# Kernel tuning notes

Hardware: AMD Instinct MI355X
Metric: run time of the kernel (lower is better)

The kernel has to match this reference:

```python
import jax, jax.numpy as jnp
import numpy as np
from jax import lax

K = 3
PAD = 1

def setup_inputs() -> dict:
    key = jax.random.key(0)
    ks = jax.random.split(key, 5)
    B, C, H, W, O = 4, 128, 128, 128, 256
    x = jax.random.normal(ks[0], (B, C, H, W), dtype=jnp.float32)
    w_off = jax.random.normal(ks[1], (3 * K * K, C, K, K), dtype=jnp.float32) * 0.05
    b_off = jnp.zeros((3 * K * K,), dtype=jnp.float32)
    w_dw = jax.random.normal(ks[2], (C, 1, K, K), dtype=jnp.float32) * 0.2
    b_dw = jnp.zeros((C,), dtype=jnp.float32)
    w_pw = jax.random.normal(ks[3], (O, C), dtype=jnp.float32) * (1.0 / np.sqrt(C))
    b_pw = jnp.zeros((O,), dtype=jnp.float32)
    return {"x": x, "w_off": w_off, "b_off": b_off, "w_dw": w_dw,
            "b_dw": b_dw, "w_pw": w_pw, "b_pw": b_pw}

def _dcn_forward(x, w_off, b_off, w_dw, b_dw, w_pw, b_pw):
    B, C, H, W = x.shape
    K2 = K * K
    # offset/mask conv (stride 1, pad 1) -> [B, 3*K*K, H, W]
    om = lax.conv_general_dilated(
        x, w_off, window_strides=(1, 1), padding=[(PAD, PAD), (PAD, PAD)],
        dimension_numbers=("NCHW", "OIHW", "NCHW")) + b_off[None, :, None, None]
    off = om[:, : 2 * K2]                      # [B, 2*K2, H, W]
    mask = jax.nn.sigmoid(om[:, 2 * K2:])      # [B, K2, H, W]
    dy = off[:, 0::2]                          # [B, K2, H, W] (y offsets)
    dx = off[:, 1::2]                          # [B, K2, H, W] (x offsets)
    # base sampling grid per kernel tap
    ky, kx = jnp.meshgrid(jnp.arange(K), jnp.arange(K), indexing="ij")
    ky = (ky.reshape(-1) - PAD).astype(x.dtype)   # [K2]
    kx = (kx.reshape(-1) - PAD).astype(x.dtype)
    py = jnp.arange(H, dtype=x.dtype)[None, None, :, None] + ky[None, :, None, None] + dy
    px = jnp.arange(W, dtype=x.dtype)[None, None, None, :] + kx[None, :, None, None] + dx
    y0 = jnp.floor(py); x0 = jnp.floor(px)
    wy = py - y0;       wx = px - x0

    def gather(yc, xc):
        # yc, xc: [B, K2, H, W] float corner coords; zero outside bounds
        valid = ((yc >= 0) & (yc < H) & (xc >= 0) & (xc < W)).astype(x.dtype)
        yi = jnp.clip(yc, 0, H - 1).astype(jnp.int32)
        xi = jnp.clip(xc, 0, W - 1).astype(jnp.int32)
        idx = yi * W + xi                       # [B, K2, H, W]
        def per_b(xb, ib):
            # xb: [C, H, W]; ib: [K2, H, W] -> [C, K2, H, W]
            return jnp.take(xb.reshape(C, -1), ib.reshape(-1), axis=1).reshape(C, K2, H, W)
        v = jax.vmap(per_b)(x, idx)             # [B, C, K2, H, W]
        return v * valid[:, None]

    val = (gather(y0, x0) * ((1 - wy) * (1 - wx))[:, None]
           + gather(y0, x0 + 1) * ((1 - wy) * wx)[:, None]
           + gather(y0 + 1, x0) * (wy * (1 - wx))[:, None]
           + gather(y0 + 1, x0 + 1) * (wy * wx)[:, None])  # [B, C, K2, H, W]
    val = val * mask[:, None]
    # depthwise deformable conv: per-channel K2 weights
    wk = w_dw.reshape(C, K2)
    out = jnp.einsum("bckhw,ck->bchw", val, wk) + b_dw[None, :, None, None]
    # pointwise 1x1 conv
    out = jnp.einsum("bchw,oc->bohw", out, w_pw) + b_pw[None, :, None, None]
    return out

def reference(x, w_off, b_off, w_dw, b_dw, w_pw, b_pw):
    return _dcn_forward(x, w_off, b_off, w_dw, b_dw, w_pw, b_pw)
```

## Files before the change

### kernel.cpp

```cpp
#include <hip/hip_runtime.h>
#include <hip/hip_bf16.h>
#include <math.h>

#define BB 4
#define CC 128
#define HH 128
#define WW 128
#define OO 256
#define HWP 16384

typedef __attribute__((ext_vector_type(8))) _Float16 half8;
typedef __attribute__((ext_vector_type(2))) _Float16 half2t;
typedef __attribute__((ext_vector_type(4))) float floatx4;

__device__ inline half2t u2h2(unsigned int u) {
  union { unsigned int i; half2t h; } z; z.i = u; return z.h;
}
__device__ inline unsigned short f2h_bits(float f) {
  union { _Float16 h; unsigned short s; } z; z.h = (_Float16)f; return z.s;
}

__device__ inline void blend2(unsigned int a00w, unsigned int a01w,
                              unsigned int a10w, unsigned int a11w,
                              half2t wt, half2t wb, float wk0, float wk1,
                              float& acc0, float& acc1) {
  unsigned int tl = __builtin_amdgcn_perm(a01w, a00w, 0x05040100u);
  unsigned int th = __builtin_amdgcn_perm(a01w, a00w, 0x07060302u);
  unsigned int bl = __builtin_amdgcn_perm(a11w, a10w, 0x05040100u);
  unsigned int bh = __builtin_amdgcn_perm(a11w, a10w, 0x07060302u);
  float v0 = __builtin_amdgcn_fdot2(u2h2(bl), wb, __builtin_amdgcn_fdot2(u2h2(tl), wt, 0.f, false), false);
  float v1 = __builtin_amdgcn_fdot2(u2h2(bh), wb, __builtin_amdgcn_fdot2(u2h2(th), wt, 0.f, false), false);
  acc0 = fmaf(v0, wk0, acc0);
  acc1 = fmaf(v1, wk1, acc1);
}

__device__ inline int om_idx(int px, int o) {
  return (((o >> 2) ^ (px & 7)) << 2) | (o & 3);
}

__global__ __launch_bounds__(256) void k_transpose(const float* __restrict__ x,
                                                   const float* __restrict__ w_off,
                                                   const float* __restrict__ w_pw,
                                                   unsigned int* __restrict__ xh32,
                                                   _Float16* __restrict__ Ah,
                                                   _Float16* __restrict__ Apw) {
  int tid = threadIdx.x;
  if (blockIdx.z == 4) {
    int e = (blockIdx.x * 128 + blockIdx.y) * 256 + tid;
    if (e < 144 * 32 * 8) {
      int kblk = e >> 8;
      int o = (e >> 3) & 31;
      int j = e & 7;
      int k = kblk * 8 + j;
      int t = k >> 7, c = k & 127;
      float w = (o < 27) ? w_off[(o * CC + c) * 9 + t] : 0.0f;
      Ah[e] = (_Float16)w;
    }
    int e2 = e - 144 * 32 * 8;
    if (e2 >= 0 && e2 < 16 * 256 * 8) {
      int cblk = e2 >> 11;
      int o = (e2 >> 3) & 255;
      int j = e2 & 7;
      Apw[e2] = (_Float16)w_pw[o * CC + cblk * 8 + j];
    }
    return;
  }
  __shared__ float tile[32][132];
  int ct = blockIdx.x;
  int h = blockIdx.y, b = blockIdx.z;
  int f4 = tid & 31;
  int cl = tid >> 5;
#pragma unroll
  for (int i = 0; i < 4; i++) {
    int c = cl + i * 8;
    float4 v = *(const float4*)(x + ((size_t)(b * CC + ct * 32 + c) * HH + h) * WW + f4 * 4);
    *(float4*)&tile[c][f4 * 4] = v;
  }
  __syncthreads();
  int cg = tid & 3;
#pragma unroll
  for (int pass = 0; pass < 2; pass++) {
    int px = pass * 64 + (tid >> 2);
    unsigned int d0, d1, d2, d3;
    d0 = (unsigned int)f2h_bits(tile[cg * 8 + 0][px]) | ((unsigned int)f2h_bits(tile[cg * 8 + 1][px]) << 16);
    d1 = (unsigned int)f2h_bits(tile[cg * 8 + 2][px]) | ((unsigned int)f2h_bits(tile[cg * 8 + 3][px]) << 16);
    d2 = (unsigned int)f2h_bits(tile[cg * 8 + 4][px]) | ((unsigned int)f2h_bits(tile[cg * 8 + 5][px]) << 16);
    d3 = (unsigned int)f2h_bits(tile[cg * 8 + 6][px]) | ((unsigned int)f2h_bits(tile[cg * 8 + 7][px]) << 16);
    uint4 z; z.x = d0; z.y = d1; z.z = d2; z.w = d3;
    *(uint4*)(xh32 + (size_t)((b * HH + h) * WW + px) * 64 + ct * 16 + cg * 4) = z;
  }
}

__global__ __launch_bounds__(256, 4) void k_fused(
    const _Float16* __restrict__ xh, const _Float16* __restrict__ Ah,
    const _Float16* __restrict__ Apw, const float* __restrict__ b_off,
    const float* __restrict__ w_dw, const float* __restrict__ b_dw,
    const float* __restrict__ bpw, float* __restrict__ out) {
  __shared__ float om_s[64][32];
  __shared__ int s_packed[64][9];
  __shared__ unsigned int s_wp[64][9][2];
  __shared__ __align__(16) _Float16 val[64][128];

  int tid = threadIdx.x;
  int bid = blockIdx.x;
  int n0 = ((bid & 7) * 128 + (bid >> 3)) * 64;
  int b = n0 >> 14;
  int h0 = (n0 >> 7) & 127;
  int wbase = n0 & 127;

  int wv = tid >> 6, lane = tid & 63;
  int n16 = lane & 15, quad = lane >> 4;

  {
    int pxb = wv * 16;
    floatx4 acc0 = {}, acc1 = {};
    half8 zz = {};
#pragma unroll
    for (int t = 0; t < 9; t++) {
      int dy = t / 3 - 1, dx = t % 3 - 1;
      int hs = h0 + dy;
      bool hok = ((unsigned)hs < HH);
      int hsc = min(max(hs, 0), HH - 1);
      int wA = wbase + pxb + n16 + dx;
      bool okA = hok && ((unsigned)wA < WW);
      int wAc = min(max(wA, 0), WW - 1);
      size_t rowoff = (size_t)((b * HH + hsc) * WW + wAc) * CC + quad * 8;
#pragma unroll
      for (int cs = 0; cs < 4; cs++) {
        half8 bh = *(const half8*)(xh + rowoff + cs * 32);
        bh = okA ? bh : zz;
        int kblk = t * 16 + cs * 4 + quad;
        const _Float16* pa = Ah + (size_t)kblk * 256 + n16 * 8;
        half8 a0 = *(const half8*)pa;
        half8 a1 = *(const half8*)(pa + 128);
        __builtin_amdgcn_s_setprio(1);
        acc0 = __builtin_amdgcn_mfma_f32_16x16x32_f16(a0, bh, acc0, 0, 0, 0);
        acc1 = __builtin_amdgcn_mfma_f32_16x16x32_f16(a1, bh, acc1, 0, 0, 0);
        __builtin_amdgcn_s_setprio(0);
      }
    }
    int px = pxb + n16;
#pragma unroll
    for (int reg = 0; reg < 4; reg++) {
      int o0 = quad * 4 + reg;
      om_s[px][om_idx(px, o0)] = acc0[reg] + b_off[o0];
      int o1 = 16 + quad * 4 + reg;
      if (o1 < 27) om_s[px][om_idx(px, o1)] = acc1[reg] + b_off[o1];
    }
  }

#pragma unroll
  for (int pass = 0; pass < 3; pass++) {
    int it = pass * 64 + lane;
    if (it < 144) {
      int pxl = it / 9;
      int k = it - pxl * 9;
      int px = wv * 16 + pxl;
      int w = wbase + px;
      float dyv = om_s[px][om_idx(px, 2 * k)];
      float dxv = om_s[px][om_idx(px, 2 * k + 1)];
      float mvv = om_s[px][om_idx(px, 18 + k)];
      mvv = 1.0f / (1.0f + __expf(-mvv));
      float py = (float)(h0 + k / 3 - 1) + dyv;
      float pxf = (float)(w + k % 3 - 1) + dxv;
      float y0f = floorf(py), x0f = floorf(pxf);
      float wy = py - y0f, wx = pxf - x0f;
      int y0 = (int)y0f, x0 = (int)x0f;
      int y1 = y0 + 1, x1 = x0 + 1;
      float v00 = (y0 >= 0 && y0 < HH && x0 >= 0 && x0 < WW) ? 1.f : 0.f;
      float v01 = (y0 >= 0 && y0 < HH && x1 >= 0 && x1 < WW) ? 1.f : 0.f;
      float v10 = (y1 >= 0 && y1 < HH && x0 >= 0 && x0 < WW) ? 1.f : 0.f;
      float v11 = (y1 >= 0 && y1 < HH && x1 >= 0 && x1 < WW) ? 1.f : 0.f;
      int y0c = min(max(y0, 0), HH - 1), y1c = min(max(y1, 0), HH - 1);
      int x0c = min(max(x0, 0), WW - 1), x1c = min(max(x1, 0), WW - 1);
      int base = ((b * HH + y0c) * WW + x0c) * CC;
      int dxf = (x1c > x0c) ? 1 : 0;
      int dyf = (y1c > y0c) ? 1 : 0;
      s_packed[px][k] = base | (dxf << 30) | (dyf << 31);
      float w00 = (1.f - wy) * (1.f - wx) * mvv * v00;
      float w01 = (1.f - wy) * wx * mvv * v01;
      float w10 = wy * (1.f - wx) * mvv * v10;
      float w11 = wy * wx * mvv * v11;
      s_wp[px][k][0] = (unsigned int)f2h_bits(w00) | ((unsigned int)f2h_bits(w01) << 16);
      s_wp[px][k][1] = (unsigned int)f2h_bits(w10) | ((unsigned int)f2h_bits(w11) << 16);
    }
  }

  {
    int c0 = lane * 2;
    const unsigned short* xs = (const unsigned short*)xh;
    float wk0[9], wk1[9];
    {
      const float* wp_ = w_dw + c0 * 9;
#pragma unroll
      for (int k = 0; k < 9; k++) { wk0[k] = wp_[k]; wk1[k] = wp_[9 + k]; }
    }
    float2 bdp = *(const float2*)(b_dw + c0);

    unsigned int A00[9], A01[9], A10[9], A11[9];
    unsigned int B00[9], B01[9], B10[9], B11[9];

    auto issue = [&](int pxl, unsigned int* c00, unsigned int* c01,
                     unsigned int* c10, unsigned int* c11) {
      int px = wv * 16 + pxl;
#pragma unroll
      for (int k = 0; k < 9; k++) {
        int pk = __builtin_amdgcn_readfirstlane(s_packed[px][k]);
        int base = (pk & 0x3FFFFFFF) + c0;
        int dxs = (pk & 0x40000000) ? CC : 0;
        int dys = (pk & 0x80000000u) ? (WW * CC) : 0;
        c00[k] = *(const unsigned int*)(xs + base);
        c01[k] = *(const unsigned int*)(xs + base + dxs);
        c10[k] = *(const unsigned int*)(xs + base + dys);
        c11[k] = *(const unsigned int*)(xs + base + dys + dxs);
      }
    };
    auto compute = [&](int pxl, const unsigned int* c00, const unsigned int* c01,
                       const unsigned int* c10, const unsigned int* c11) {
      int px = wv * 16 + pxl;
      float a0 = 0.f, a1 = 0.f;
#pragma unroll
      for (int k = 0; k < 9; k++) {
        uint2 w2 = *(const uint2*)&s_wp[px][k][0];
        blend2(c00[k], c01[k], c10[k], c11[k], u2h2(w2.x), u2h2(w2.y),
               wk0[k], wk1[k], a0, a1);
      }
      unsigned int d = (unsigned int)f2h_bits(a0 + bdp.x) |
                       ((unsigned int)f2h_bits(a1 + bdp.y) << 16);
      int su = (lane >> 2) ^ (px & 7);
      *(unsigned int*)((char*)&val[px][0] + su * 16 + (lane & 3) * 4) = d;
    };

    issue(0, A00, A01, A10, A11);
#pragma unroll
    for (int i = 0; i < 16; i += 2) {
      issue(i + 1, B00, B01, B10, B11);
      compute(i, A00, A01, A10, A11);
      if (i + 2 < 16) issue(i + 2, A00, A01, A10, A11);
      compute(i + 1, B00, B01, B10, B11);
    }
  }
  __syncthreads();

  {
    int obase = wv * 64;
#pragma unroll
    for (int mh = 0; mh < 2; mh++) {
      floatx4 acc[2][4] = {};
#pragma unroll
      for (int cs = 0; cs < 4; cs++) {
        half8 af[2], bf[4];
#pragma unroll
        for (int mf = 0; mf < 2; mf++) {
          const _Float16* pa = Apw + ((size_t)(cs * 4 + quad) * 256 + obase + (mh * 2 + mf) * 16 + n16) * 8;
          af[mf] = *(const half8*)pa;
        }
#pragma unroll
        for (int nf = 0; nf < 4; nf++) {
          int row = nf * 16 + n16;
          int su = (cs * 4 + quad) ^ (row & 7);
          bf[nf] = *(const half8*)&val[row][su * 8];
        }
        __builtin_amdgcn_s_setprio(1);
#pragma unroll
        for (int mf = 0; mf < 2; mf++)
#pragma unroll
          for (int nf = 0; nf < 4; nf++)
            acc[mf][nf] = __builtin_amdgcn_mfma_f32_16x16x32_f16(af[mf], bf[nf], acc[mf][nf], 0, 0, 0);
        __builtin_amdgcn_s_setprio(0);
      }
#pragma unroll
      for (int mf = 0; mf < 2; mf++) {
#pragma unroll
        for (int reg = 0; reg < 4; reg++) {
          int o = obase + (mh * 2 + mf) * 16 + quad * 4 + reg;
          float bo = bpw[o];
#pragma unroll
          for (int nf = 0; nf < 4; nf++) {
            int n = n0 + nf * 16 + n16;
            int hw = n & 16383;
            out[((size_t)(b * OO + o) << 14) + hw] = acc[mf][nf][reg] + bo;
          }
        }
      }
    }
  }
}

extern "C" void kernel_launch(void* const* d_in, const int* in_sizes, int n_in,
                              void* d_out, int out_size, void* d_ws, size_t ws_size,
                              hipStream_t stream) {
  const float* x     = (const float*)d_in[0];
  const float* w_off = (const float*)d_in[1];
  const float* b_off = (const float*)d_in[2];
  const float* w_dw  = (const float*)d_in[3];
  const float* b_dw  = (const float*)d_in[4];
  const float* w_pw  = (const float*)d_in[5];
  const float* b_pw  = (const float*)d_in[6];
  float* out = (float*)d_out;
  float* ws  = (float*)d_ws;

  _Float16* xh  = (_Float16*)ws;
  _Float16* Ah  = (_Float16*)((char*)ws + 16777216);
  _Float16* Apw = Ah + 36864;

  k_transpose<<<dim3(4, 128, 5), 256, 0, stream>>>(x, w_off, w_pw,
                                                   (unsigned int*)xh, Ah, Apw);
  k_fused<<<1024, 256, 0, stream>>>(xh, Ah, Apw, b_off, w_dw, b_dw, b_pw, out);
}
```

Before: 161.9 us.

## Halve fused tile to 32 pixels, restructure transpose to write full 256B rows

The fused kernel now handles 32 pixels per block instead of 64 and launches twice as many blocks. Only two waves compute the offset conv, behind an added barrier. The gather loop drops its double-buffered issue/compute pipeline, and the pointwise GEMM now does one pass of 4x2 MFMA tiles. The transpose kernel reads pairs of channels over half-row tiles with an XOR-swizzled LDS layout, so each block writes complete 128-channel pixel rows. The aim is more parallelism and lower per-block register/LDS pressure, at the cost of idle waves in the offset stage and less load/compute overlap in the gather.

Measured after the change: 157.7 us. 2.6% less time.

```diff
diff --git a/kernel.cpp b/kernel.cpp
--- a/kernel.cpp
+++ b/kernel.cpp
@@ -45,8 +45,9 @@
                                                    _Float16* __restrict__ Ah,
                                                    _Float16* __restrict__ Apw) {
   int tid = threadIdx.x;
-  if (blockIdx.z == 4) {
-    int e = (blockIdx.x * 128 + blockIdx.y) * 256 + tid;
+  int bid = blockIdx.x;
+  if (bid >= 1024) {
+    int e = (bid - 1024) * 256 + tid;
     if (e < 144 * 32 * 8) {
       int kblk = e >> 8;
       int o = (e >> 3) & 31;
@@ -65,29 +66,36 @@
     }
     return;
   }
-  __shared__ float tile[32][132];
-  int ct = blockIdx.x;
-  int h = blockIdx.y, b = blockIdx.z;
-  int f4 = tid & 31;
-  int cl = tid >> 5;
+  __shared__ __align__(16) unsigned int tile32[64][64];
+  int half = bid & 1;
+  int h = (bid >> 1) & 127;
+  int b = bid >> 8;
+  int wq = tid & 15;
+  int cb = tid >> 4;
 #pragma unroll
   for (int i = 0; i < 4; i++) {
-    int c = cl + i * 8;
-    float4 v = *(const float4*)(x + ((size_t)(b * CC + ct * 32 + c) * HH + h) * WW + f4 * 4);
-    *(float4*)&tile[c][f4 * 4] = v;
+    int c0 = i * 32 + cb * 2;
+    const float* p0 = x + ((size_t)(b * CC + c0) * HH + h) * WW + half * 64 + wq * 4;
+    float4 v0 = *(const float4*)p0;
+    float4 v1 = *(const float4*)(p0 + HWP);
+    const float* f0 = &v0.x;
+    const float* f1 = &v1.x;
+    int cp = i * 16 + cb;
+    int su = (cp >> 2) ^ wq;
+#pragma unroll
+    for (int j = 0; j < 4; j++) {
+      unsigned int pk = (unsigned int)f2h_bits(f0[j]) | ((unsigned int)f2h_bits(f1[j]) << 16);
+      tile32[wq * 4 + j][su * 4 + (cp & 3)] = pk;
+    }
   }
   __syncthreads();
-  int cg = tid & 3;
-#pragma unroll
-  for (int pass = 0; pass < 2; pass++) {
-    int px = pass * 64 + (tid >> 2);
-    unsigned int d0, d1, d2, d3;
-    d0 = (unsigned int)f2h_bits(tile[cg * 8 + 0][px]) | ((unsigned int)f2h_bits(tile[cg * 8 + 1][px]) << 16);
-    d1 = (unsigned int)f2h_bits(tile[cg * 8 + 2][px]) | ((unsigned int)f2h_bits(tile[cg * 8 + 3][px]) << 16);
-    d2 = (unsigned int)f2h_bits(tile[cg * 8 + 4][px]) | ((unsigned int)f2h_bits(tile[cg * 8 + 5][px]) << 16);
-    d3 = (unsigned int)f2h_bits(tile[cg * 8 + 6][px]) | ((unsigned int)f2h_bits(tile[cg * 8 + 7][px]) << 16);
-    uint4 z; z.x = d0; z.y = d1; z.z = d2; z.w = d3;
-    *(uint4*)(xh32 + (size_t)((b * HH + h) * WW + px) * 64 + ct * 16 + cg * 4) = z;
+  int cg = tid & 15;
+#pragma unroll
+  for (int p = 0; p < 4; p++) {
+    int w = p * 16 + (tid >> 4);
+    int su = cg ^ ((w >> 2) & 15);
+    uint4 v = *(const uint4*)&tile32[w][su * 4];
+    *(uint4*)(xh32 + (size_t)((b * HH + h) * WW + half * 64 + w) * 64 + cg * 4) = v;
   }
 }
 
@@ -96,14 +104,14 @@
     const _Float16* __restrict__ Apw, const float* __restrict__ b_off,
     const float* __restrict__ w_dw, const float* __restrict__ b_dw,
     const float* __restrict__ bpw, float* __restrict__ out) {
-  __shared__ float om_s[64][32];
-  __shared__ int s_packed[64][9];
-  __shared__ unsigned int s_wp[64][9][2];
-  __shared__ __align__(16) _Float16 val[64][128];
+  __shared__ float om_s[32][32];
+  __shared__ int s_packed[32][9];
+  __shared__ unsigned int s_wp[32][9][2];
+  __shared__ __align__(16) _Float16 val[32][128];
 
   int tid = threadIdx.x;
   int bid = blockIdx.x;
-  int n0 = ((bid & 7) * 128 + (bid >> 3)) * 64;
+  int n0 = ((bid & 7) * 256 + (bid >> 3)) * 32;
   int b = n0 >> 14;
   int h0 = (n0 >> 7) & 127;
   int wbase = n0 & 127;
@@ -111,7 +119,7 @@
   int wv = tid >> 6, lane = tid & 63;
   int n16 = lane & 15, quad = lane >> 4;
 
-  {
+  if (wv < 2) {
     int pxb = wv * 16;
     floatx4 acc0 = {}, acc1 = {};
     half8 zz = {};
@@ -148,14 +156,15 @@
       if (o1 < 27) om_s[px][om_idx(px, o1)] = acc1[reg] + b_off[o1];
     }
   }
-
-#pragma unroll
-  for (int pass = 0; pass < 3; pass++) {
+  __syncthreads();
+
+#pragma unroll
+  for (int pass = 0; pass < 2; pass++) {
     int it = pass * 64 + lane;
-    if (it < 144) {
+    if (it < 72) {
       int pxl = it / 9;
       int k = it - pxl * 9;
-      int px = wv * 16 + pxl;
+      int px = wv * 8 + pxl;
       int w = wbase + px;
       float dyv = om_s[px][om_idx(px, 2 * k)];
       float dxv = om_s[px][om_idx(px, 2 * k + 1)];
@@ -197,90 +206,72 @@
     }
     float2 bdp = *(const float2*)(b_dw + c0);
 
-    unsigned int A00[9], A01[9], A10[9], A11[9];
-    unsigned int B00[9], B01[9], B10[9], B11[9];
-
-    auto issue = [&](int pxl, unsigned int* c00, unsigned int* c01,
-                     unsigned int* c10, unsigned int* c11) {
-      int px = wv * 16 + pxl;
+#pragma unroll
+    for (int p = 0; p < 8; p++) {
+      int px = wv * 8 + p;
+      unsigned int C00[9], C01[9], C10[9], C11[9];
 #pragma unroll
       for (int k = 0; k < 9; k++) {
         int pk = __builtin_amdgcn_readfirstlane(s_packed[px][k]);
         int base = (pk & 0x3FFFFFFF) + c0;
         int dxs = (pk & 0x40000000) ? CC : 0;
         int dys = (pk & 0x80000000u) ? (WW * CC) : 0;
-        c00[k] = *(const unsigned int*)(xs + base);
-        c01[k] = *(const unsigned int*)(xs + base + dxs);
-        c10[k] = *(const unsigned int*)(xs + base + dys);
-        c11[k] = *(const unsigned int*)(xs + base + dys + dxs);
-      }
-    };
-    auto compute = [&](int pxl, const unsigned int* c00, const unsigned int* c01,
-                       const unsigned int* c10, const unsigned int* c11) {
-      int px = wv * 16 + pxl;
+        C00[k] = *(const unsigned int*)(xs + base);
+        C01[k] = *(const unsigned int*)(xs + base + dxs);
+        C10[k] = *(const unsigned int*)(xs + base + dys);
+        C11[k] = *(const unsigned int*)(xs + base + dys + dxs);
+      }
       float a0 = 0.f, a1 = 0.f;
 #pragma unroll
       for (int k = 0; k < 9; k++) {
         uint2 w2 = *(const uint2*)&s_wp[px][k][0];
-        blend2(c00[k], c01[k], c10[k], c11[k], u2h2(w2.x), u2h2(w2.y),
+        blend2(C00[k], C01[k], C10[k], C11[k], u2h2(w2.x), u2h2(w2.y),
                wk0[k], wk1[k], a0, a1);
       }
       unsigned int d = (unsigned int)f2h_bits(a0 + bdp.x) |
                        ((unsigned int)f2h_bits(a1 + bdp.y) << 16);
       int su = (lane >> 2) ^ (px & 7);
       *(unsigned int*)((char*)&val[px][0] + su * 16 + (lane & 3) * 4) = d;
-    };
-
-    issue(0, A00, A01, A10, A11);
-#pragma unroll
-    for (int i = 0; i < 16; i += 2) {
-      issue(i + 1, B00, B01, B10, B11);
-      compute(i, A00, A01, A10, A11);
-      if (i + 2 < 16) issue(i + 2, A00, A01, A10, A11);
-      compute(i + 1, B00, B01, B10, B11);
     }
   }
   __syncthreads();
 
   {
     int obase = wv * 64;
-#pragma unroll
-    for (int mh = 0; mh < 2; mh++) {
-      floatx4 acc[2][4] = {};
-#pragma unroll
-      for (int cs = 0; cs < 4; cs++) {
-        half8 af[2], bf[4];
-#pragma unroll
-        for (int mf = 0; mf < 2; mf++) {
-          const _Float16* pa = Apw + ((size_t)(cs * 4 + quad) * 256 + obase + (mh * 2 + mf) * 16 + n16) * 8;
-          af[mf] = *(const half8*)pa;
-        }
-#pragma unroll
-        for (int nf = 0; nf < 4; nf++) {
-          int row = nf * 16 + n16;
-          int su = (cs * 4 + quad) ^ (row & 7);
-          bf[nf] = *(const half8*)&val[row][su * 8];
-        }
-        __builtin_amdgcn_s_setprio(1);
-#pragma unroll
-        for (int mf = 0; mf < 2; mf++)
-#pragma unroll
-          for (int nf = 0; nf < 4; nf++)
-            acc[mf][nf] = __builtin_amdgcn_mfma_f32_16x16x32_f16(af[mf], bf[nf], acc[mf][nf], 0, 0, 0);
-        __builtin_amdgcn_s_setprio(0);
-      }
-#pragma unroll
-      for (int mf = 0; mf < 2; mf++) {
-#pragma unroll
-        for (int reg = 0; reg < 4; reg++) {
-          int o = obase + (mh * 2 + mf) * 16 + quad * 4 + reg;
-          float bo = bpw[o];
-#pragma unroll
-          for (int nf = 0; nf < 4; nf++) {
-            int n = n0 + nf * 16 + n16;
-            int hw = n & 16383;
-            out[((size_t)(b * OO + o) << 14) + hw] = acc[mf][nf][reg] + bo;
-          }
+    floatx4 acc[4][2] = {};
+#pragma unroll
+    for (int cs = 0; cs < 4; cs++) {
+      half8 af[4], bf[2];
+#pragma unroll
+      for (int mf = 0; mf < 4; mf++) {
+        const _Float16* pa = Apw + ((size_t)(cs * 4 + quad) * 256 + obase + mf * 16 + n16) * 8;
+        af[mf] = *(const half8*)pa;
+      }
+#pragma unroll
+      for (int nf = 0; nf < 2; nf++) {
+        int row = nf * 16 + n16;
+        int su = (cs * 4 + quad) ^ (row & 7);
+        bf[nf] = *(const half8*)&val[row][su * 8];
+      }
+      __builtin_amdgcn_s_setprio(1);
+#pragma unroll
+      for (int mf = 0; mf < 4; mf++)
+#pragma unroll
+        for (int nf = 0; nf < 2; nf++)
+          acc[mf][nf] = __builtin_amdgcn_mfma_f32_16x16x32_f16(af[mf], bf[nf], acc[mf][nf], 0, 0, 0);
+      __builtin_amdgcn_s_setprio(0);
+    }
+#pragma unroll
+    for (int mf = 0; mf < 4; mf++) {
+#pragma unroll
+      for (int reg = 0; reg < 4; reg++) {
+        int o = obase + mf * 16 + quad * 4 + reg;
+        float bo = bpw[o];
+#pragma unroll
+        for (int nf = 0; nf < 2; nf++) {
+          int n = n0 + nf * 16 + n16;
+          int hw = n & 16383;
+          out[((size_t)(b * OO + o) << 14) + hw] = acc[mf][nf][reg] + bo;
         }
       }
     }
@@ -304,7 +295,7 @@
   _Float16* Ah  = (_Float16*)((char*)ws + 16777216);
   _Float16* Apw = Ah + 36864;
 
-  k_transpose<<<dim3(4, 128, 5), 256, 0, stream>>>(x, w_off, w_pw,
-                                                   (unsigned int*)xh, Ah, Apw);
-  k_fused<<<1024, 256, 0, stream>>>(xh, Ah, Apw, b_off, w_dw, b_dw, b_pw, out);
-}
+  k_transpose<<<1536, 256, 0, stream>>>(x, w_off, w_pw,
+                                        (unsigned int*)xh, Ah, Apw);
+  k_fused<<<2048, 256, 0, stream>>>(xh, Ah, Apw, b_off, w_dw, b_dw, b_pw, out);
+}
```
